# Kernel tuning notes

Hardware: AMD Instinct MI355X
Metric: run time of the kernel (lower is better)

## Reference

```python
import jax, jax.numpy as jnp
import numpy as np

C0, C1, ED, H, L, K = 128, 32, 64, 4, 2, 16
RADIUS = 16.0
EPS = 1e-6


def _ln(x, g, b):
    m = jnp.mean(x, -1, keepdims=True)
    v = jnp.var(x, -1, keepdims=True)
    return (x - m) * jax.lax.rsqrt(v + 1e-5) * g + b


def _gather_nodes(x, idx):
    # x [B,N,...], idx [B,N,K] -> [B,N,K,...]
    return jax.vmap(lambda xb, ib: xb[ib])(x, idx)


def _gather_pairs(e, idx):
    # e [B,N,N,ED], idx [B,N,K] -> [B,N,K,ED]  (batched_index_select on dim=2)
    return jax.vmap(lambda eb, ib: jnp.take_along_axis(eb, ib[..., None], axis=1))(e, idx)


def _fiber_norm(f0, f1, g0, b0, g1, b1):
    # deg-0: LayerNorm + gelu; deg-1: phase-preserving norm on channel magnitudes
    f0n = jax.nn.gelu(_ln(f0, g0, b0))
    n1 = jnp.linalg.norm(f1, axis=-1)                       # [B,N,C1]
    f1n = f1 / (n1 + EPS)[..., None] * jax.nn.gelu(_ln(n1, g1, b1))[..., None]
    return f0n, f1n


def _tfn_kv(f0j, f1j, y1, r, WA, WB):
    # Equivariant TFN edge kernel: paths 0->0(l=0), 1->0(l=1), 0->1(l=1),
    # 1->1(l=0), 1->1(l=1, cross), 1->1(l=2, traceless Y2) with radial gates r.
    r1, r2, r3, r4, r5, r6 = jnp.split(
        r, [C0, C0 + C1, 2 * C0 + C1, 2 * C0 + 2 * C1, 2 * C0 + 3 * C1], axis=-1)
    dot1 = jnp.einsum('bnkcm,bnkm->bnkc', f1j, y1)          # [B,N,K,C1]
    in0 = jnp.concatenate([r1 * f0j, r2 * dot1], -1)        # [B,N,K,C0+C1]
    k0 = jnp.einsum('oc,bnkc->bnko', WA, in0)               # [B,N,K,C0]
    p3 = (r3 * f0j)[..., None] * y1[..., None, :]           # [B,N,K,C0,3]
    p4 = r4[..., None] * f1j
    p5 = r5[..., None] * jnp.cross(f1j, y1[..., None, :])
    p6 = r6[..., None] * (y1[..., None, :] * dot1[..., None] - f1j / 3.0)
    in1 = jnp.concatenate([p3, p4, p5, p6], axis=-2)        # [B,N,K,C0+3*C1,3]
    k1 = jnp.einsum('oc,bnkcm->bnkom', WB, in1)             # [B,N,K,C1,3]
    return k0, k1


def reference(node_feats, pair_feats, coords, eln_g, eln_b, Wi0, Wi1,
              ln0_g, ln0_b, n1_g, n1_b, Wq0, Wq1, WrK, WrV, WkA, WkB, WvA, WvB,
              Wb, Wo0, Wo1, alpha_attn, lnf0_g, lnf0_b, nf1_g, nf1_b,
              Wf0a, Wf0b, Wf1a, Wf1b, alpha_ff, Wp0, Wp1):
    B, N = node_feats.shape[:2]
    Na, CA, Cc, Oo = [coords[..., i, :] for i in range(4)]          # each [B,N,3]
    f1_in = jnp.stack([Na, Cc, Oo], axis=-2) - CA[..., None, :]     # [B,N,3,3]
    # kNN graph on CA coords (exclude self), radius mask at 16A
    d2 = jnp.sum((CA[:, :, None] - CA[:, None, :]) ** 2, -1)        # [B,N,N]
    d2 = d2 + jnp.eye(N, dtype=d2.dtype) * 1e9
    nv, idx = jax.lax.top_k(-d2, K)                                 # idx [B,N,K]
    dist = jnp.sqrt(jnp.maximum(-nv, 0.0))
    mask = dist <= RADIUS
    rel_pos = _gather_nodes(CA, idx) - CA[:, :, None]               # [B,N,K,3]
    rel_b = jax.lax.stop_gradient(rel_pos)                          # basis on detached rel_pos
    y1 = rel_b / (jnp.linalg.norm(rel_b, axis=-1, keepdims=True) + EPS)
    edges = _ln(_gather_pairs(pair_feats, idx), eln_g, eln_b)       # [B,N,K,ED]
    # project in
    f0 = jnp.einsum('oc,bnc->bno', Wi0, node_feats)                 # [B,N,C0]
    f1 = jnp.einsum('oc,bncm->bnom', Wi1, f1_in)                    # [B,N,C1,3]
    dh0, dh1 = C0 // H, C1 // H
    scale = 1.0 / np.sqrt(dh0 + 3 * dh1)
    for l in range(L):
        # ---- attention block (prenorm -> TFN attention -> rezero residual)
        x0, x1 = _fiber_norm(f0, f1, ln0_g[l], ln0_b[l], n1_g[l], n1_b[l])
        q0 = jnp.einsum('oc,bnc->bno', Wq0[l], x0)
        q1 = jnp.einsum('oc,bncm->bnom', Wq1[l], x1)
        x0j = _gather_nodes(x0, idx)                                # [B,N,K,C0]
        x1j = _gather_nodes(x1, idx)                                # [B,N,K,C1,3]
        rk = jnp.einsum('re,bnke->bnkr', WrK[l], edges)
        rv = jnp.einsum('re,bnke->bnkr', WrV[l], edges)
        k0, k1 = _tfn_kv(x0j, x1j, y1, rk, WkA[l], WkB[l])
        v0, v1 = _tfn_kv(x0j, x1j, y1, rv, WvA[l], WvB[l])
        q0h = q0.reshape(B, N, H, dh0)
        q1h = q1.reshape(B, N, H, dh1, 3)
        k0h = k0.reshape(B, N, K, H, dh0)
        k1h = k1.reshape(B, N, K, H, dh1, 3)
        v0h = v0.reshape(B, N, K, H, dh0)
        v1h = v1.reshape(B, N, K, H, dh1, 3)
        logits = (jnp.einsum('bnhc,bnkhc->bnhk', q0h, k0h)
                  + jnp.einsum('bnhcm,bnkhcm->bnhk', q1h, k1h)) * scale
        logits = logits + jnp.einsum('he,bnke->bnhk', Wb[l], edges)
        logits = jnp.where(mask[:, :, None, :], logits, -1e9)
        attn = jax.nn.softmax(logits, axis=-1)
        o0 = jnp.einsum('bnhk,bnkhc->bnhc', attn, v0h).reshape(B, N, C0)
        o1 = jnp.einsum('bnhk,bnkhcm->bnhcm', attn, v1h).reshape(B, N, C1, 3)
        f0 = f0 + alpha_attn[l] * jnp.einsum('oc,bnc->bno', Wo0[l], o0)
        f1 = f1 + alpha_attn[l] * jnp.einsum('oc,bncm->bnom', Wo1[l], o1)
        # ---- fiber feedforward (prenorm -> FF -> rezero residual)
        x0, x1 = _fiber_norm(f0, f1, lnf0_g[l], lnf0_b[l], nf1_g[l], nf1_b[l])
        h0 = jnp.einsum('oh,bnh->bno', Wf0b[l],
                        jax.nn.gelu(jnp.einsum('hc,bnc->bnh', Wf0a[l], x0)))
        h1 = jnp.einsum('hc,bncm->bnhm', Wf1a[l], x1)
        nh = jnp.linalg.norm(h1, axis=-1)
        h1 = h1 * (jax.nn.gelu(nh) / (nh + EPS))[..., None]
        h1 = jnp.einsum('oh,bnhm->bnom', Wf1b[l], h1)
        f0 = f0 + alpha_ff[l] * h0
        f1 = f1 + alpha_ff[l] * h1
    # project out + _to_output
    node_out = jnp.einsum('oc,bnc->bno', Wp0, f0)                   # [B,N,128]
    coords_out = CA[:, :, None, :] + jnp.einsum('oc,bncm->bnom', Wp1, f1)  # [B,N,3,3]
    return node_out, coords_out


def setup_inputs() -> dict:
    key = jax.random.key(0)
    ks = iter(jax.random.split(key, 64))
    def rn(shape, scale=1.0):
        return (jax.random.normal(next(ks), shape) * scale).astype(jnp.float32)
    B, N = 1, 1024
    RC = 2 * C0 + 4 * C1
    ca = jnp.cumsum(rn((B, N, 3), 1.5), axis=1)          # protein-like chain
    coords = ca[:, :, None, :] + rn((B, N, 4, 3), 0.5)
    inp = dict(
        node_feats=rn((B, N, 128)),
        pair_feats=rn((B, N, N, ED)),
        coords=coords,
        eln_g=jnp.ones((ED,), jnp.float32), eln_b=jnp.zeros((ED,), jnp.float32),
        Wi0=rn((C0, 128), 128 ** -0.5), Wi1=rn((C1, 3), 3 ** -0.5),
        ln0_g=jnp.ones((L, C0), jnp.float32), ln0_b=jnp.zeros((L, C0), jnp.float32),
        n1_g=jnp.ones((L, C1), jnp.float32), n1_b=jnp.zeros((L, C1), jnp.float32),
        Wq0=rn((L, C0, C0), C0 ** -0.5), Wq1=rn((L, C1, C1), C1 ** -0.5),
        WrK=rn((L, RC, ED), ED ** -0.5), WrV=rn((L, RC, ED), ED ** -0.5),
        WkA=rn((L, C0, C0 + C1), (C0 + C1) ** -0.5),
        WkB=rn((L, C1, C0 + 3 * C1), (C0 + 3 * C1) ** -0.5),
        WvA=rn((L, C0, C0 + C1), (C0 + C1) ** -0.5),
        WvB=rn((L, C1, C0 + 3 * C1), (C0 + 3 * C1) ** -0.5),
        Wb=rn((L, H, ED), ED ** -0.5),
        Wo0=rn((L, C0, C0), C0 ** -0.5), Wo1=rn((L, C1, C1), C1 ** -0.5),
        alpha_attn=jnp.full((L,), 0.5, jnp.float32),
        lnf0_g=jnp.ones((L, C0), jnp.float32), lnf0_b=jnp.zeros((L, C0), jnp.float32),
        nf1_g=jnp.ones((L, C1), jnp.float32), nf1_b=jnp.zeros((L, C1), jnp.float32),
        Wf0a=rn((L, 4 * C0, C0), C0 ** -0.5), Wf0b=rn((L, C0, 4 * C0), (4 * C0) ** -0.5),
        Wf1a=rn((L, 4 * C1, C1), C1 ** -0.5), Wf1b=rn((L, C1, 4 * C1), (4 * C1) ** -0.5),
        alpha_ff=jnp.full((L,), 0.5, jnp.float32),
        Wp0=rn((128, C0), C0 ** -0.5), Wp1=rn((3, C1), C1 ** -0.5),
    )
    return inp
```

## Files before the change

kernel.cpp:

```cpp
#include <hip/hip_runtime.h>
#include <hip/hip_bf16.h>
#include <math.h>

static constexpr int NN  = 1024;
static constexpr int KK  = 16;
static constexpr int C0c = 128;
static constexpr int C1c = 32;
static constexpr int EDc = 64;
static constexpr int Lc  = 2;
static constexpr int ENUM = NN * KK;
static constexpr int PL   = NN * C1c;
static constexpr int X1HS = NN * 32;
#define SCALE_ATTN 0.13363062095621219f

typedef __attribute__((ext_vector_type(8))) short s8v;
typedef __attribute__((ext_vector_type(4))) float f4v;

__device__ __forceinline__ float wsum64(float v) {
    for (int o = 32; o > 0; o >>= 1) v += __shfl_xor(v, o);
    return v;
}
__device__ __forceinline__ float gsum16(float v) {
    for (int o = 8; o > 0; o >>= 1) v += __shfl_xor(v, o, 16);
    return v;
}
__device__ __forceinline__ float gmax16(float v) {
    for (int o = 8; o > 0; o >>= 1) v = fmaxf(v, __shfl_xor(v, o, 16));
    return v;
}
__device__ __forceinline__ float gelu_f(float x) {
    float x3 = x * x * x;
    return 0.5f * x * (1.0f + tanhf(0.7978845608028654f * (x + 0.044715f * x3)));
}
__device__ __forceinline__ unsigned short f2bf(float x) {
    union { float f; unsigned int u; } v; v.f = x;
    unsigned int r = v.u + 0x7fffu + ((v.u >> 16) & 1u);
    return (unsigned short)(r >> 16);
}
__device__ __forceinline__ float bf2f(unsigned short u) {
    union { float f; unsigned int i; } v; v.i = ((unsigned int)u) << 16;
    return v.f;
}
__device__ __forceinline__ s8v ld8(const unsigned short* p) { return *(const s8v*)p; }
__device__ __forceinline__ f4v mfma16(s8v a, s8v b, f4v c) {
    return __builtin_amdgcn_mfma_f32_16x16x32_bf16(a, b, c, 0, 0, 0);
}

struct CvJob { const float* s; unsigned short* d; int n; };
struct CvJobs { CvJob j[20]; int n; int total; };

__global__ __launch_bounds__(256) void setup_kernel(CvJobs cj, int cvb,
                                                    const float* __restrict__ coords,
                                                    int* __restrict__ idx,
                                                    float* __restrict__ maskf,
                                                    float* __restrict__ y1,
                                                    const float* __restrict__ Wi1,
                                                    float* __restrict__ f1p) {
    __shared__ float ca[NN * 3];
    const int tid = threadIdx.x;
    const int bx = blockIdx.x;
    if (bx < cvb) {
        int g = bx * 256 + tid;
        if (g >= cj.total) return;
        for (int i = 0; i < cj.n; ++i) {
            int n = cj.j[i].n;
            if (g < n) { cj.j[i].d[g] = f2bf(cj.j[i].s[g]); return; }
            g -= n;
        }
        return;
    }
    if (bx < cvb + 256) {
        for (int f = tid; f < NN * 3; f += 256) {
            int i = f / 3, m = f % 3;
            ca[f] = coords[(i * 4 + 1) * 3 + m];
        }
        __syncthreads();
        const int wid = tid >> 6, lane = tid & 63;
        const int n = (bx - cvb) * 4 + wid;
        const float cx = ca[n * 3 + 0], cy = ca[n * 3 + 1], cz = ca[n * 3 + 2];
        float d[16];
#pragma unroll
        for (int s = 0; s < 16; ++s) {
            int i = s * 64 + lane;
            float dx = cx - ca[i * 3 + 0], dy = cy - ca[i * 3 + 1], dz = cz - ca[i * 3 + 2];
            float d2 = dx * dx + dy * dy + dz * dz;
            d[s] = (i == n) ? 1e9f : d2;
        }
        for (int t = 0; t < KK; ++t) {
            float best = 1e30f; int bi = 0;
#pragma unroll
            for (int s = 0; s < 16; ++s) {
                int i = s * 64 + lane;
                float v = d[s];
                if (v < best || (v == best && i < bi)) { best = v; bi = i; }
            }
#pragma unroll
            for (int o = 32; o > 0; o >>= 1) {
                float ov = __shfl_xor(best, o);
                int   oi = __shfl_xor(bi, o);
                if (ov < best || (ov == best && oi < bi)) { best = ov; bi = oi; }
            }
            const int j = bi;
            if (lane == 0) {
                idx[n * KK + t] = j;
                float dist = sqrtf(best);
                maskf[n * KK + t] = (dist <= 16.0f) ? 1.0f : 0.0f;
                float rx = ca[j * 3 + 0] - cx, ry = ca[j * 3 + 1] - cy, rz = ca[j * 3 + 2] - cz;
                float nrm = sqrtf(rx * rx + ry * ry + rz * rz) + 1e-6f;
                y1[(n * KK + t) * 3 + 0] = rx / nrm;
                y1[(n * KK + t) * 3 + 1] = ry / nrm;
                y1[(n * KK + t) * 3 + 2] = rz / nrm;
            }
            const int js = j >> 6, jl = j & 63;
#pragma unroll
            for (int s = 0; s < 16; ++s)
                if (s == js && jl == lane) d[s] = 2e30f;
        }
        return;
    }
    int g = (bx - cvb - 256) * 256 + tid;
    if (g >= NN * 32) return;
    int n = g >> 5, c = g & 31;
    float w0 = Wi1[c * 3 + 0], w1 = Wi1[c * 3 + 1], w2 = Wi1[c * 3 + 2];
#pragma unroll
    for (int m = 0; m < 3; ++m) {
        float cav = coords[(n * 4 + 1) * 3 + m];
        float a0 = coords[(n * 4 + 0) * 3 + m] - cav;
        float a1 = coords[(n * 4 + 2) * 3 + m] - cav;
        float a2 = coords[(n * 4 + 3) * 3 + m] - cav;
        f1p[m * PL + n * 32 + c] = w0 * a0 + w1 * a1 + w2 * a2;
    }
}

__global__ __launch_bounds__(256) void edge_f0_kernel(const float* __restrict__ pair,
                                                      const int* __restrict__ idx,
                                                      const float* __restrict__ g,
                                                      const float* __restrict__ b,
                                                      const float* __restrict__ Wb,
                                                      unsigned short* __restrict__ edges_h,
                                                      float* __restrict__ biasb,
                                                      const unsigned short* __restrict__ nf_h,
                                                      const unsigned short* __restrict__ Wi0_h,
                                                      float* __restrict__ f0) {
    const int t = threadIdx.x, wid = t >> 6, lane = t & 63;
    if (blockIdx.x < ENUM / 4) {
        const int e = blockIdx.x * 4 + wid;
        const int n = e >> 4;
        const int j = idx[e];
        float v = pair[((size_t)n * NN + j) * EDc + lane];
        float m = wsum64(v) * (1.0f / 64.0f);
        float d = v - m;
        float var = wsum64(d * d) * (1.0f / 64.0f);
        float nv = d * rsqrtf(var + 1e-5f) * g[lane] + b[lane];
        edges_h[e * EDc + lane] = f2bf(nv);
#pragma unroll
        for (int l = 0; l < 2; ++l)
#pragma unroll
            for (int h = 0; h < 4; ++h) {
                float tt = wsum64(nv * Wb[(l * 4 + h) * 64 + lane]);
                if (lane == 0) biasb[(size_t)l * ENUM * 4 + e * 4 + h] = tt;
            }
        return;
    }
    int rel = blockIdx.x - ENUM / 4;
    const int mt = rel & 7, ntc = rel >> 3;
    const int m0 = mt * 128 + wid * 32, n0 = ntc * 32;
    const int c16 = lane & 15, g8 = (lane >> 4) * 8, g4 = (lane >> 4) * 4;
    f4v acc[2][2];
#pragma unroll
    for (int a = 0; a < 2; ++a)
#pragma unroll
        for (int bq = 0; bq < 2; ++bq) acc[a][bq] = f4v{0.f, 0.f, 0.f, 0.f};
    const unsigned short* Ap = nf_h + (size_t)(m0 + c16) * 128 + g8;
    const unsigned short* Bp = Wi0_h + (size_t)(n0 + c16) * 128 + g8;
#pragma unroll
    for (int kc = 0; kc < 128; kc += 32) {
        s8v a0 = ld8(Ap + kc);
        s8v a1 = ld8(Ap + 16 * 128 + kc);
        s8v b0 = ld8(Bp + kc);
        s8v b1 = ld8(Bp + 16 * 128 + kc);
        acc[0][0] = mfma16(a0, b0, acc[0][0]);
        acc[0][1] = mfma16(a0, b1, acc[0][1]);
        acc[1][0] = mfma16(a1, b0, acc[1][0]);
        acc[1][1] = mfma16(a1, b1, acc[1][1]);
    }
#pragma unroll
    for (int fm = 0; fm < 2; ++fm)
#pragma unroll
        for (int r = 0; r < 4; ++r) {
            const int m = m0 + fm * 16 + g4 + r;
#pragma unroll
            for (int fn = 0; fn < 2; ++fn)
                f0[(size_t)m * 128 + n0 + fn * 16 + c16] = acc[fm][fn][r];
        }
}

__global__ __launch_bounds__(256) void fnorm1_kernel(const float* __restrict__ f0,
                                                     const float* __restrict__ f1p,
                                                     const float* __restrict__ g0,
                                                     const float* __restrict__ b0,
                                                     const float* __restrict__ g1,
                                                     const float* __restrict__ b1,
                                                     unsigned short* __restrict__ x0h,
                                                     unsigned short* __restrict__ x1h) {
    const int wid = threadIdx.x >> 6, lane = threadIdx.x & 63;
    const int n = blockIdx.x * 4 + wid;
    float va = f0[n * 128 + lane], vb = f0[n * 128 + lane + 64];
    float m = wsum64(va + vb) * (1.0f / 128.0f);
    float da = va - m, db = vb - m;
    float var = wsum64(da * da + db * db) * (1.0f / 128.0f);
    float rs = rsqrtf(var + 1e-5f);
    x0h[n * 128 + lane]      = f2bf(gelu_f(da * rs * g0[lane] + b0[lane]));
    x0h[n * 128 + lane + 64] = f2bf(gelu_f(db * rs * g0[lane + 64] + b0[lane + 64]));
    int c = lane & 31;
    float h0 = f1p[0 * PL + n * 32 + c];
    float h1 = f1p[1 * PL + n * 32 + c];
    float h2 = f1p[2 * PL + n * 32 + c];
    float n1 = sqrtf(h0 * h0 + h1 * h1 + h2 * h2);
    float ms = wsum64(n1) * (1.0f / 64.0f);
    float dd = n1 - ms;
    float vv = wsum64(dd * dd) * (1.0f / 64.0f);
    float sc = gelu_f(dd * rsqrtf(vv + 1e-5f) * g1[c] + b1[c]) / (n1 + 1e-6f);
    if (lane < 32) {
        x1h[0 * X1HS + n * 32 + c] = f2bf(h0 * sc);
        x1h[1 * X1HS + n * 32 + c] = f2bf(h1 * sc);
        x1h[2 * X1HS + n * 32 + c] = f2bf(h2 * sc);
    }
}

static constexpr int LS_IN0 = 0;
static constexpr int LS_INU = 64 * 168;
static constexpr int LS_INW = LS_INU + 64 * 136;
static constexpr int LS_X0  = LS_INW + 3 * 64 * 104;
static constexpr int LS_X1  = LS_X0 + 64 * 128;
static constexpr int LS_Y   = LS_X1 + 3 * 64 * 32;
static constexpr int EKV_LDS2 = LS_Y * 2 + 64 * 3 * 4;

__global__ __launch_bounds__(512) void edge_kv2(
    const unsigned short* __restrict__ edges_h,
    const unsigned short* __restrict__ WrK, const unsigned short* __restrict__ WrV,
    const unsigned short* __restrict__ WkA, const unsigned short* __restrict__ WvA,
    const unsigned short* __restrict__ WkB, const unsigned short* __restrict__ WvB,
    const unsigned short* __restrict__ x0h, const unsigned short* __restrict__ x1h,
    const int* __restrict__ idx, const float* __restrict__ y1,
    unsigned short* __restrict__ k0h, unsigned short* __restrict__ v0h,
    unsigned short* __restrict__ uKh, unsigned short* __restrict__ uVh,
    unsigned short* __restrict__ k1ph, unsigned short* __restrict__ v1ph,
    const unsigned short* __restrict__ Wq0l, const unsigned short* __restrict__ Wq1l,
    float* __restrict__ q0, float* __restrict__ q1p) {
    extern __shared__ unsigned short lsm[];
    const int t = threadIdx.x, w = t >> 6, l = t & 63;
    const int c16 = l & 15, g8 = (l >> 4) * 8, g4 = (l >> 4) * 4;
    const int bid = blockIdx.x;
    if (bid < 256) {
        unsigned short* in0L = lsm + LS_IN0;
        unsigned short* inUL = lsm + LS_INU;
        unsigned short* inWL = lsm + LS_INW;
        unsigned short* x0L  = lsm + LS_X0;
        unsigned short* x1L  = lsm + LS_X1;
        float* yL = (float*)(lsm + LS_Y);
        const int e0 = bid * 64;
        for (int c = t; c < 1024; c += 512) {
            int row = c >> 4, sub = c & 15;
            int j = idx[e0 + row];
            *(s8v*)&x0L[row * 128 + sub * 8] = ld8(x0h + (size_t)j * 128 + sub * 8);
        }
        for (int c = t; c < 768; c += 512) {
            int plane = c >> 8, rem = c & 255;
            int row = rem >> 2, sub = rem & 3;
            int j = idx[e0 + row];
            *(s8v*)&x1L[(plane * 64 + row) * 32 + sub * 8] =
                ld8(x1h + (size_t)plane * X1HS + (size_t)j * 32 + sub * 8);
        }
        if (t < 192) yL[t] = y1[e0 * 3 + t];
        __syncthreads();
#pragma unroll 1
        for (int s = 0; s < 2; ++s) {
            const unsigned short* Wr = s ? WrV : WrK;
            const unsigned short* WA = s ? WvA : WkA;
            const unsigned short* WB = s ? WvB : WkB;
            unsigned short* K0o = s ? v0h : k0h;
            unsigned short* Uo  = s ? uVh : uKh;
            unsigned short* K1o = s ? v1ph : k1ph;
#pragma unroll 1
            for (int ti = w; ti < 24; ti += 8) {
                const int esub = ti & 1, rt = ti >> 1;
                const int e0w = e0 + esub * 32, r0 = rt * 32;
                f4v acc[2][2];
#pragma unroll
                for (int a = 0; a < 2; ++a)
#pragma unroll
                    for (int bq = 0; bq < 2; ++bq) acc[a][bq] = f4v{0.f, 0.f, 0.f, 0.f};
#pragma unroll
                for (int kc = 0; kc < 64; kc += 32) {
                    s8v a0 = ld8(edges_h + (size_t)(e0w + c16) * 64 + kc + g8);
                    s8v a1 = ld8(edges_h + (size_t)(e0w + 16 + c16) * 64 + kc + g8);
                    s8v b0 = ld8(Wr + (size_t)(r0 + c16) * 64 + kc + g8);
                    s8v b1 = ld8(Wr + (size_t)(r0 + 16 + c16) * 64 + kc + g8);
                    acc[0][0] = mfma16(a0, b0, acc[0][0]);
                    acc[0][1] = mfma16(a0, b1, acc[0][1]);
                    acc[1][0] = mfma16(a1, b0, acc[1][0]);
                    acc[1][1] = mfma16(a1, b1, acc[1][1]);
                }
#pragma unroll
                for (int fm = 0; fm < 2; ++fm)
#pragma unroll
                    for (int r = 0; r < 4; ++r) {
                        const int el = esub * 32 + fm * 16 + g4 + r;
                        float ya = yL[el * 3 + 0], yb = yL[el * 3 + 1], yc = yL[el * 3 + 2];
#pragma unroll
                        for (int fn = 0; fn < 2; ++fn) {
                            const float av = acc[fm][fn][r];
                            const int col = r0 + fn * 16 + c16;
                            if (r0 < 128) {
                                in0L[el * 168 + col] = f2bf(av * bf2f(x0L[el * 128 + col]));
                            } else if (r0 < 160) {
                                int c = col - 128;
                                float d1 = bf2f(x1L[(0 * 64 + el) * 32 + c]) * ya
                                         + bf2f(x1L[(1 * 64 + el) * 32 + c]) * yb
                                         + bf2f(x1L[(2 * 64 + el) * 32 + c]) * yc;
                                in0L[el * 168 + col] = f2bf(av * d1);
                            } else if (r0 < 288) {
                                int c = col - 160;
                                inUL[el * 136 + c] = f2bf(av * bf2f(x0L[el * 128 + c]));
                            } else {
                                int c = (r0 < 320) ? (col - 288) : (r0 < 352) ? (col - 320) : (col - 352);
                                float fx = bf2f(x1L[(0 * 64 + el) * 32 + c]);
                                float fy = bf2f(x1L[(1 * 64 + el) * 32 + c]);
                                float fz = bf2f(x1L[(2 * 64 + el) * 32 + c]);
                                float w0, w1, w2; int off;
                                if (r0 < 320) {
                                    off = 0; w0 = av * fx; w1 = av * fy; w2 = av * fz;
                                } else if (r0 < 352) {
                                    off = 32;
                                    w0 = av * (fy * yc - fz * yb);
                                    w1 = av * (fz * ya - fx * yc);
                                    w2 = av * (fx * yb - fy * ya);
                                } else {
                                    off = 64;
                                    float d1 = fx * ya + fy * yb + fz * yc;
                                    w0 = av * (ya * d1 - fx * (1.0f / 3.0f));
                                    w1 = av * (yb * d1 - fy * (1.0f / 3.0f));
                                    w2 = av * (yc * d1 - fz * (1.0f / 3.0f));
                                }
                                inWL[0 * 64 * 104 + el * 104 + off + c] = f2bf(w0);
                                inWL[1 * 64 * 104 + el * 104 + off + c] = f2bf(w1);
                                inWL[2 * 64 * 104 + el * 104 + off + c] = f2bf(w2);
                            }
                        }
                    }
            }
            __syncthreads();
#pragma unroll 1
            for (int ti = w; ti < 16; ti += 8) {
                const unsigned short* Ab; const unsigned short* Bb;
                unsigned short* Cb;
                int apit, K, ldb, ldcq, esub;
                if (ti < 8) {
                    esub = ti & 1; int nt = ti >> 1;
                    Ab = in0L; apit = 168; K = 160;
                    Bb = WA + (size_t)(nt * 32) * 160; ldb = 160;
                    Cb = K0o + (size_t)(e0 + esub * 32) * 128 + nt * 32; ldcq = 128;
                } else if (ti < 10) {
                    esub = ti - 8;
                    Ab = inUL; apit = 136; K = 128; Bb = WB; ldb = 224;
                    Cb = Uo + (size_t)(e0 + esub * 32) * 32; ldcq = 32;
                } else {
                    int id = ti - 10; int m = id >> 1; esub = id & 1;
                    Ab = inWL + m * 64 * 104; apit = 104; K = 96;
                    Bb = WB + 128; ldb = 224;
                    Cb = K1o + ((size_t)m * ENUM + e0 + esub * 32) * 32; ldcq = 32;
                }
                const int m0l = esub * 32;
                f4v acc[2][2];
#pragma unroll
                for (int a = 0; a < 2; ++a)
#pragma unroll
                    for (int bq = 0; bq < 2; ++bq) acc[a][bq] = f4v{0.f, 0.f, 0.f, 0.f};
                for (int kc = 0; kc < K; kc += 32) {
                    s8v a0 = *(const s8v*)&Ab[(m0l + c16) * apit + kc + g8];
                    s8v a1 = *(const s8v*)&Ab[(m0l + 16 + c16) * apit + kc + g8];
                    s8v b0 = ld8(Bb + (size_t)c16 * ldb + kc + g8);
                    s8v b1 = ld8(Bb + (size_t)(16 + c16) * ldb + kc + g8);
                    acc[0][0] = mfma16(a0, b0, acc[0][0]);
                    acc[0][1] = mfma16(a0, b1, acc[0][1]);
                    acc[1][0] = mfma16(a1, b0, acc[1][0]);
                    acc[1][1] = mfma16(a1, b1, acc[1][1]);
                }
#pragma unroll
                for (int fm = 0; fm < 2; ++fm)
#pragma unroll
                    for (int r = 0; r < 4; ++r) {
                        const int lr = fm * 16 + g4 + r;
#pragma unroll
                        for (int fn = 0; fn < 2; ++fn)
                            Cb[(size_t)lr * ldcq + fn * 16 + c16] = f2bf(acc[fm][fn][r]);
                    }
            }
            __syncthreads();
        }
        return;
    }
    const int wt = (bid - 256) * 8 + w;
    const unsigned short* A; const unsigned short* B;
    float* C; int K, lda2, m0, n0, ldc2;
    if (wt < 128) {
        int rowt = wt >> 2, colt = wt & 3;
        A = x0h; B = Wq0l; C = q0;
        K = 128; lda2 = 128; ldc2 = 128;
        m0 = rowt * 32; n0 = colt * 32;
    } else {
        int k = wt - 128;
        int pl = k >> 5, rowt = k & 31;
        A = x1h + (size_t)pl * X1HS; B = Wq1l; C = q1p + (size_t)pl * PL;
        K = 32; lda2 = 32; ldc2 = 32;
        m0 = rowt * 32; n0 = 0;
    }
    f4v acc[2][2];
#pragma unroll
    for (int a = 0; a < 2; ++a)
#pragma unroll
        for (int bq = 0; bq < 2; ++bq) acc[a][bq] = f4v{0.f, 0.f, 0.f, 0.f};
    const unsigned short* Ap = A + (size_t)(m0 + c16) * lda2 + g8;
    const unsigned short* Bp = B + (size_t)(n0 + c16) * lda2 + g8;
    for (int kc = 0; kc < K; kc += 32) {
        s8v a0 = ld8(Ap + kc);
        s8v a1 = ld8(Ap + 16 * lda2 + kc);
        s8v b0 = ld8(Bp + kc);
        s8v b1 = ld8(Bp + 16 * lda2 + kc);
        acc[0][0] = mfma16(a0, b0, acc[0][0]);
        acc[0][1] = mfma16(a0, b1, acc[0][1]);
        acc[1][0] = mfma16(a1, b0, acc[1][0]);
        acc[1][1] = mfma16(a1, b1, acc[1][1]);
    }
#pragma unroll
    for (int fm = 0; fm < 2; ++fm)
#pragma unroll
        for (int r = 0; r < 4; ++r) {
            const int m = m0 + fm * 16 + g4 + r;
#pragma unroll
            for (int fn = 0; fn < 2; ++fn)
                C[(size_t)m * ldc2 + n0 + fn * 16 + c16] = acc[fm][fn][r];
        }
}

__global__ __launch_bounds__(256) void attn_core(const float* __restrict__ q0,
                                                 const float* __restrict__ q1p,
                                                 const unsigned short* __restrict__ k0h,
                                                 const unsigned short* __restrict__ k1ph,
                                                 const unsigned short* __restrict__ v0h,
                                                 const unsigned short* __restrict__ v1ph,
                                                 const unsigned short* __restrict__ uKh,
                                                 const unsigned short* __restrict__ uVh,
                                                 const float* __restrict__ biasb,
                                                 const float* __restrict__ maskf,
                                                 const float* __restrict__ y1,
                                                 unsigned short* __restrict__ o0h,
                                                 unsigned short* __restrict__ o1h) {
    __shared__ float q0s[4][128];
    __shared__ float q1s[4][96];
    __shared__ float attns[4][64];
    const int wid = threadIdx.x >> 6, lane = threadIdx.x & 63;
    const int n = blockIdx.x * 4 + wid;
    q0s[wid][lane]      = q0[n * 128 + lane];
    q0s[wid][lane + 64] = q0[n * 128 + lane + 64];
    if (lane < 32) {
#pragma unroll
        for (int m = 0; m < 3; ++m) q1s[wid][m * 32 + lane] = q1p[m * PL + n * 32 + lane];
    }
    __syncthreads();
    {
        const int h = lane >> 4, k = lane & 15;
        const int e = n * KK + k;
        float acc = 0.f;
        const unsigned short* kr = k0h + (size_t)e * 128 + h * 32;
#pragma unroll
        for (int c8 = 0; c8 < 4; ++c8) {
            s8v kv = ld8(kr + c8 * 8);
#pragma unroll
            for (int j = 0; j < 8; ++j)
                acc += q0s[wid][h * 32 + c8 * 8 + j] * bf2f((unsigned short)kv[j]);
        }
        s8v uv = ld8(uKh + (size_t)e * 32 + h * 8);
#pragma unroll
        for (int m = 0; m < 3; ++m) {
            float yv = y1[e * 3 + m];
            s8v k1v = ld8(k1ph + ((size_t)m * ENUM + e) * 32 + h * 8);
#pragma unroll
            for (int c = 0; c < 8; ++c)
                acc += q1s[wid][m * 32 + h * 8 + c] *
                       (bf2f((unsigned short)k1v[c]) + bf2f((unsigned short)uv[c]) * yv);
        }
        acc = acc * SCALE_ATTN + biasb[e * 4 + h];
        if (maskf[e] == 0.0f) acc = -1e9f;
        float mx = gmax16(acc);
        float ex = expf(acc - mx);
        float sm = gsum16(ex);
        attns[wid][lane] = ex / sm;
    }
    __syncthreads();
    const int g = lane & 15, kq = lane >> 4;
    {
        float o[8] = {};
        const float* aw = &attns[wid][(g >> 2) * 16];
#pragma unroll
        for (int kk2 = 0; kk2 < 4; ++kk2) {
            int kk = kq * 4 + kk2;
            float a = aw[kk];
            s8v v = ld8(v0h + (size_t)(n * KK + kk) * 128 + g * 8);
#pragma unroll
            for (int j = 0; j < 8; ++j) o[j] += a * bf2f((unsigned short)v[j]);
        }
#pragma unroll
        for (int j = 0; j < 8; ++j) {
            o[j] += __shfl_xor(o[j], 16);
            o[j] += __shfl_xor(o[j], 32);
        }
        if (kq == 0) {
            s8v r;
#pragma unroll
            for (int j = 0; j < 8; ++j) r[j] = (short)f2bf(o[j]);
            *(s8v*)&o0h[(size_t)n * 128 + g * 8] = r;
        }
    }
    {
        float o[8] = {};
        const int plane = g >> 2, cg = g & 3;
        if (g < 12) {
            const float* aw = &attns[wid][cg * 16];
#pragma unroll
            for (int kk2 = 0; kk2 < 4; ++kk2) {
                int kk = kq * 4 + kk2;
                int e2 = n * KK + kk;
                float a = aw[kk];
                float yv = y1[e2 * 3 + plane];
                s8v v = ld8(v1ph + ((size_t)plane * ENUM + e2) * 32 + cg * 8);
                s8v u = ld8(uVh + (size_t)e2 * 32 + cg * 8);
#pragma unroll
                for (int j = 0; j < 8; ++j)
                    o[j] += a * (bf2f((unsigned short)v[j]) + bf2f((unsigned short)u[j]) * yv);
            }
        }
#pragma unroll
        for (int j = 0; j < 8; ++j) {
            o[j] += __shfl_xor(o[j], 16);
            o[j] += __shfl_xor(o[j], 32);
        }
        if (kq == 0 && g < 12) {
            s8v r;
#pragma unroll
            for (int j = 0; j < 8; ++j) r[j] = (short)f2bf(o[j]);
            *(s8v*)&o1h[((size_t)plane * NN + n) * 32 + cg * 8] = r;
        }
    }
}

template <int MODE>
__global__ __launch_bounds__(512) void fused_post(
    const unsigned short* __restrict__ o0h, const unsigned short* __restrict__ o1h,
    float* __restrict__ f0, float* __restrict__ f1p,
    const unsigned short* __restrict__ Wo0h, const unsigned short* __restrict__ Wo1h,
    const unsigned short* __restrict__ Wf0ah, const unsigned short* __restrict__ Wf0bh,
    const unsigned short* __restrict__ Wf1ah, const unsigned short* __restrict__ Wf1bh,
    const float* __restrict__ alA, const float* __restrict__ alF,
    const float* __restrict__ lnf0_g, const float* __restrict__ lnf0_b,
    const float* __restrict__ nf1_g, const float* __restrict__ nf1_b,
    const float* __restrict__ ln0n_g, const float* __restrict__ ln0n_b,
    const float* __restrict__ n1n_g, const float* __restrict__ n1n_b,
    unsigned short* __restrict__ x0h, unsigned short* __restrict__ x1h,
    const unsigned short* __restrict__ Wp0h, const float* __restrict__ Wp1,
    const float* __restrict__ coords, float* __restrict__ out) {
    __shared__ float f0s[16][132];
    __shared__ float f1s[3][16][36];
    __shared__ unsigned short x0s[16][136];
    __shared__ float x1s[3][16][36];
    __shared__ unsigned short hs[16][520];
    __shared__ unsigned short h1b[3][16][136];
    const int t = threadIdx.x, w = t >> 6, l = t & 63;
    const int c16 = l & 15, g8 = (l >> 4) * 8, g4 = (l >> 4) * 4;
    const int n0 = blockIdx.x * 16;
    const float aA = alA[0], aF = alF[0];

    {
        f4v acc = f4v{0.f, 0.f, 0.f, 0.f};
        const unsigned short* Ap = o0h + (size_t)(n0 + c16) * 128 + g8;
#pragma unroll
        for (int kc = 0; kc < 128; kc += 32) {
            s8v a = ld8(Ap + kc);
            s8v b = ld8(Wo0h + (size_t)(w * 16 + c16) * 128 + g8 + kc);
            acc = mfma16(a, b, acc);
        }
        int colg = w * 16 + c16;
#pragma unroll
        for (int r = 0; r < 4; ++r) {
            int row = g4 + r;
            f0s[row][colg] = f0[(size_t)(n0 + row) * 128 + colg] + aA * acc[r];
        }
    }
#pragma unroll
    for (int it = 0; it < 3; ++it) {
        int g = t + it * 512;
        int c = g & 31, node = (g >> 5) & 15, m = g >> 9;
        float a = 0.f;
        const unsigned short* wrow = Wo1h + c * 32;
        const unsigned short* orow = o1h + ((size_t)m * NN + n0 + node) * 32;
#pragma unroll
        for (int cc = 0; cc < 32; ++cc) a += bf2f(wrow[cc]) * bf2f(orow[cc]);
        f1s[m][node][c] = f1p[(size_t)m * PL + (n0 + node) * 32 + c] + aA * a;
    }
    __syncthreads();
    for (int i = 0; i < 2; ++i) {
        int row = w * 2 + i;
        float v0 = f0s[row][l], v1 = f0s[row][l + 64];
        float mn = wsum64(v0 + v1) * (1.0f / 128.0f);
        float d0 = v0 - mn, d1 = v1 - mn;
        float var = wsum64(d0 * d0 + d1 * d1) * (1.0f / 128.0f);
        float rs = rsqrtf(var + 1e-5f);
        x0s[row][l]      = f2bf(gelu_f(d0 * rs * lnf0_g[l] + lnf0_b[l]));
        x0s[row][l + 64] = f2bf(gelu_f(d1 * rs * lnf0_g[l + 64] + lnf0_b[l + 64]));
    }
    if (t < 256) {
        int node = t >> 4, sub = t & 15;
        float p[2][3], n1v[2];
#pragma unroll
        for (int q = 0; q < 2; ++q) {
            int c = sub + q * 16;
            p[q][0] = f1s[0][node][c]; p[q][1] = f1s[1][node][c]; p[q][2] = f1s[2][node][c];
            n1v[q] = sqrtf(p[q][0]*p[q][0] + p[q][1]*p[q][1] + p[q][2]*p[q][2]);
        }
        float s = gsum16(n1v[0] + n1v[1]);
        float mn = s * (1.0f / 32.0f);
        float d0 = n1v[0] - mn, d1 = n1v[1] - mn;
        float vv = gsum16(d0 * d0 + d1 * d1);
        float rs = rsqrtf(vv * (1.0f / 32.0f) + 1e-5f);
#pragma unroll
        for (int q = 0; q < 2; ++q) {
            int c = sub + q * 16;
            float sc = gelu_f((n1v[q] - mn) * rs * nf1_g[c] + nf1_b[c]) / (n1v[q] + 1e-6f);
            x1s[0][node][c] = p[q][0] * sc;
            x1s[1][node][c] = p[q][1] * sc;
            x1s[2][node][c] = p[q][2] * sc;
        }
    }
    __syncthreads();
    {
        f4v acc[4];
#pragma unroll
        for (int i = 0; i < 4; ++i) acc[i] = f4v{0.f,0.f,0.f,0.f};
#pragma unroll
        for (int kc = 0; kc < 128; kc += 32) {
            s8v a = *(const s8v*)&x0s[c16][kc + g8];
#pragma unroll
            for (int tt = 0; tt < 4; ++tt) {
                s8v b = ld8(Wf0ah + (size_t)((w * 4 + tt) * 16 + c16) * 128 + g8 + kc);
                acc[tt] = mfma16(a, b, acc[tt]);
            }
        }
#pragma unroll
        for (int tt = 0; tt < 4; ++tt) {
            int colg = (w * 4 + tt) * 16 + c16;
#pragma unroll
            for (int r = 0; r < 4; ++r) hs[g4 + r][colg] = f2bf(gelu_f(acc[tt][r]));
        }
    }
#pragma unroll
    for (int it = 0; it < 4; ++it) {
        int g = t + it * 512;
        int r = g & 127, node = g >> 7;
        float a0 = 0.f, a1 = 0.f, a2 = 0.f;
        const unsigned short* wrow = Wf1ah + r * 32;
#pragma unroll
        for (int c = 0; c < 32; ++c) {
            float wv = bf2f(wrow[c]);
            a0 += wv * x1s[0][node][c];
            a1 += wv * x1s[1][node][c];
            a2 += wv * x1s[2][node][c];
        }
        float nh = sqrtf(a0 * a0 + a1 * a1 + a2 * a2);
        float sc = gelu_f(nh) / (nh + 1e-6f);
        h1b[0][node][r] = f2bf(a0 * sc);
        h1b[1][node][r] = f2bf(a1 * sc);
        h1b[2][node][r] = f2bf(a2 * sc);
    }
    __syncthreads();
    {
        f4v acc = f4v{0.f, 0.f, 0.f, 0.f};
#pragma unroll 4
        for (int kc = 0; kc < 512; kc += 32) {
            s8v a = *(const s8v*)&hs[c16][kc + g8];
            s8v b = ld8(Wf0bh + (size_t)(w * 16 + c16) * 512 + g8 + kc);
            acc = mfma16(a, b, acc);
        }
        int colg = w * 16 + c16;
#pragma unroll
        for (int r = 0; r < 4; ++r) {
            int row = g4 + r;
            float v = f0s[row][colg] + aF * acc[r];
            f0s[row][colg] = v;
            f0[(size_t)(n0 + row) * 128 + colg] = v;
        }
    }
#pragma unroll
    for (int it = 0; it < 3; ++it) {
        int g = t + it * 512;
        int c = g & 31, node = (g >> 5) & 15, m = g >> 9;
        float a = 0.f;
        const unsigned short* wrow = Wf1bh + c * 128;
#pragma unroll 8
        for (int r = 0; r < 128; ++r) a += bf2f(wrow[r]) * bf2f(h1b[m][node][r]);
        float v = f1s[m][node][c] + aF * a;
        f1s[m][node][c] = v;
        f1p[(size_t)m * PL + (n0 + node) * 32 + c] = v;
    }
    __syncthreads();
    if (MODE == 0) {
        for (int i = 0; i < 2; ++i) {
            int row = w * 2 + i;
            float v0 = f0s[row][l], v1 = f0s[row][l + 64];
            float mn = wsum64(v0 + v1) * (1.0f / 128.0f);
            float d0 = v0 - mn, d1 = v1 - mn;
            float var = wsum64(d0 * d0 + d1 * d1) * (1.0f / 128.0f);
            float rs = rsqrtf(var + 1e-5f);
            x0h[(size_t)(n0 + row) * 128 + l]      = f2bf(gelu_f(d0 * rs * ln0n_g[l] + ln0n_b[l]));
            x0h[(size_t)(n0 + row) * 128 + l + 64] = f2bf(gelu_f(d1 * rs * ln0n_g[l + 64] + ln0n_b[l + 64]));
        }
        if (t < 256) {
            int node = t >> 4, sub = t & 15;
            float p[2][3], n1v[2];
#pragma unroll
            for (int q = 0; q < 2; ++q) {
                int c = sub + q * 16;
                p[q][0] = f1s[0][node][c]; p[q][1] = f1s[1][node][c]; p[q][2] = f1s[2][node][c];
                n1v[q] = sqrtf(p[q][0]*p[q][0] + p[q][1]*p[q][1] + p[q][2]*p[q][2]);
            }
            float s = gsum16(n1v[0] + n1v[1]);
            float mn = s * (1.0f / 32.0f);
            float d0 = n1v[0] - mn, d1 = n1v[1] - mn;
            float vv = gsum16(d0 * d0 + d1 * d1);
            float rs = rsqrtf(vv * (1.0f / 32.0f) + 1e-5f);
#pragma unroll
            for (int q = 0; q < 2; ++q) {
                int c = sub + q * 16;
                float sc = gelu_f((n1v[q] - mn) * rs * n1n_g[c] + n1n_b[c]) / (n1v[q] + 1e-6f);
                x1h[(size_t)0 * X1HS + (n0 + node) * 32 + c] = f2bf(p[q][0] * sc);
                x1h[(size_t)1 * X1HS + (n0 + node) * 32 + c] = f2bf(p[q][1] * sc);
                x1h[(size_t)2 * X1HS + (n0 + node) * 32 + c] = f2bf(p[q][2] * sc);
            }
        }
    } else {
#pragma unroll
        for (int it = 0; it < 4; ++it) {
            int g = t + it * 512;
            int row = g >> 7, col = g & 127;
            x0s[row][col] = f2bf(f0s[row][col]);
        }
        __syncthreads();
        f4v acc = f4v{0.f, 0.f, 0.f, 0.f};
#pragma unroll
        for (int kc = 0; kc < 128; kc += 32) {
            s8v a = *(const s8v*)&x0s[c16][kc + g8];
            s8v b = ld8(Wp0h + (size_t)(w * 16 + c16) * 128 + g8 + kc);
            acc = mfma16(a, b, acc);
        }
        int colg = w * 16 + c16;
#pragma unroll
        for (int r = 0; r < 4; ++r)
            out[(size_t)(n0 + g4 + r) * 128 + colg] = acc[r];
        if (t < 144) {
            int node = t / 9, rr = t % 9, o = rr / 3, m = rr % 3;
            float a = coords[((size_t)(n0 + node) * 4 + 1) * 3 + m];
            for (int c = 0; c < 32; ++c) a += Wp1[o * 32 + c] * f1s[m][node][c];
            out[NN * 128 + ((size_t)(n0 + node) * 3 + o) * 3 + m] = a;
        }
    }
}

extern "C" void kernel_launch(void* const* d_in, const int* in_sizes, int n_in,
                              void* d_out, int out_size, void* d_ws, size_t ws_size,
                              hipStream_t stream) {
    (void)in_sizes; (void)n_in; (void)out_size; (void)ws_size;
    const float* node_feats = (const float*)d_in[0];
    const float* pair       = (const float*)d_in[1];
    const float* coords     = (const float*)d_in[2];
    const float* eln_g      = (const float*)d_in[3];
    const float* eln_b      = (const float*)d_in[4];
    const float* Wi0        = (const float*)d_in[5];
    const float* Wi1        = (const float*)d_in[6];
    const float* ln0_g      = (const float*)d_in[7];
    const float* ln0_b      = (const float*)d_in[8];
    const float* n1_g       = (const float*)d_in[9];
    const float* n1_b       = (const float*)d_in[10];
    const float* Wq0        = (const float*)d_in[11];
    const float* Wq1        = (const float*)d_in[12];
    const float* WrK        = (const float*)d_in[13];
    const float* WrV        = (const float*)d_in[14];
    const float* WkA        = (const float*)d_in[15];
    const float* WkB        = (const float*)d_in[16];
    const float* WvA        = (const float*)d_in[17];
    const float* WvB        = (const float*)d_in[18];
    const float* Wb         = (const float*)d_in[19];
    const float* Wo0        = (const float*)d_in[20];
    const float* Wo1        = (const float*)d_in[21];
    const float* alpha_attn = (const float*)d_in[22];
    const float* lnf0_g     = (const float*)d_in[23];
    const float* lnf0_b     = (const float*)d_in[24];
    const float* nf1_g      = (const float*)d_in[25];
    const float* nf1_b      = (const float*)d_in[26];
    const float* Wf0a       = (const float*)d_in[27];
    const float* Wf0b       = (const float*)d_in[28];
    const float* Wf1a       = (const float*)d_in[29];
    const float* Wf1b       = (const float*)d_in[30];
    const float* alpha_ff   = (const float*)d_in[31];
    const float* Wp0        = (const float*)d_in[32];
    const float* Wp1        = (const float*)d_in[33];
    float* out = (float*)d_out;

    float* ws = (float*)d_ws;
    size_t off = 0;
    int*   idx   = (int*)(ws + off); off += NN * KK;
    float* maskf = ws + off;         off += NN * KK;
    float* y1    = ws + off;         off += NN * KK * 3;
    float* f0    = ws + off;         off += NN * C0c;
    float* f1p   = ws + off;         off += 3 * PL;
    float* q0    = ws + off;         off += NN * C0c;
    float* q1p   = ws + off;         off += 3 * PL;
    float* biasb = ws + off;         off += (size_t)2 * ENUM * 4;
    off = (off + 3) & ~(size_t)3;
    unsigned short* up = (unsigned short*)(ws + off);
    size_t uo = 0;
    unsigned short* edges_h = up + uo; uo += (size_t)ENUM * 64;
    unsigned short* x0h     = up + uo; uo += (size_t)NN * 128;
    unsigned short* x1h     = up + uo; uo += (size_t)3 * X1HS;
    unsigned short* nf_h    = up + uo; uo += (size_t)NN * 128;
    unsigned short* k0h     = up + uo; uo += (size_t)ENUM * 128;
    unsigned short* v0h     = up + uo; uo += (size_t)ENUM * 128;
    unsigned short* uKh     = up + uo; uo += (size_t)ENUM * 32;
    unsigned short* uVh     = up + uo; uo += (size_t)ENUM * 32;
    unsigned short* k1ph    = up + uo; uo += (size_t)3 * ENUM * 32;
    unsigned short* v1ph    = up + uo; uo += (size_t)3 * ENUM * 32;
    unsigned short* o0h     = up + uo; uo += (size_t)NN * 128;
    unsigned short* o1h     = up + uo; uo += (size_t)3 * NN * 32;
    unsigned short* WrK_h   = up + uo; uo += 2 * 24576;
    unsigned short* WrV_h   = up + uo; uo += 2 * 24576;
    unsigned short* WkA_h   = up + uo; uo += 2 * 20480;
    unsigned short* WvA_h   = up + uo; uo += 2 * 20480;
    unsigned short* WkB_h   = up + uo; uo += 2 * 7168;
    unsigned short* WvB_h   = up + uo; uo += 2 * 7168;
    unsigned short* Wq0_h   = up + uo; uo += 2 * 16384;
    unsigned short* Wq1_h   = up + uo; uo += 2 * 1024;
    unsigned short* Wo0_h   = up + uo; uo += 2 * 16384;
    unsigned short* Wo1_h   = up + uo; uo += 2 * 1024;
    unsigned short* Wf0a_h  = up + uo; uo += 2 * 65536;
    unsigned short* Wf0b_h  = up + uo; uo += 2 * 65536;
    unsigned short* Wf1a_h  = up + uo; uo += 2 * 4096;
    unsigned short* Wf1b_h  = up + uo; uo += 2 * 4096;
    unsigned short* Wp0_h   = up + uo; uo += 16384;
    unsigned short* Wi0_h   = up + uo; uo += 16384;

    CvJobs cj; cj.n = 17;
    cj.j[0]  = {WrK,  WrK_h,  2 * 24576};
    cj.j[1]  = {WrV,  WrV_h,  2 * 24576};
    cj.j[2]  = {WkA,  WkA_h,  2 * 20480};
    cj.j[3]  = {WvA,  WvA_h,  2 * 20480};
    cj.j[4]  = {WkB,  WkB_h,  2 * 7168};
    cj.j[5]  = {WvB,  WvB_h,  2 * 7168};
    cj.j[6]  = {Wq0,  Wq0_h,  2 * 16384};
    cj.j[7]  = {Wq1,  Wq1_h,  2 * 1024};
    cj.j[8]  = {Wo0,  Wo0_h,  2 * 16384};
    cj.j[9]  = {Wo1,  Wo1_h,  2 * 1024};
    cj.j[10] = {Wf0a, Wf0a_h, 2 * 65536};
    cj.j[11] = {Wf0b, Wf0b_h, 2 * 65536};
    cj.j[12] = {Wf1a, Wf1a_h, 2 * 4096};
    cj.j[13] = {Wf1b, Wf1b_h, 2 * 4096};
    cj.j[14] = {Wp0,  Wp0_h,  16384};
    cj.j[15] = {Wi0,  Wi0_h,  16384};
    cj.j[16] = {node_feats, nf_h, NN * 128};
    cj.total = 2*24576*2 + 2*20480*2 + 2*7168*2 + 2*16384 + 2*1024 + 2*16384
             + 2*1024 + 2*65536*2 + 2*4096*2 + 16384 + 16384 + NN*128;
    const int cvb = (cj.total + 255) / 256;

    setup_kernel<<<cvb + 256 + 128, 256, 0, stream>>>(cj, cvb, coords, idx, maskf, y1, Wi1, f1p);
    edge_f0_kernel<<<ENUM / 4 + 32, 256, 0, stream>>>(pair, idx, eln_g, eln_b, Wb,
                                                      edges_h, biasb, nf_h, Wi0_h, f0);
    fnorm1_kernel<<<NN / 4, 256, 0, stream>>>(f0, f1p, ln0_g, ln0_b, n1_g, n1_b, x0h, x1h);

    for (int l = 0; l < Lc; ++l) {
        edge_kv2<<<284, 512, EKV_LDS2, stream>>>(
            edges_h,
            WrK_h + (size_t)l * 24576, WrV_h + (size_t)l * 24576,
            WkA_h + (size_t)l * 20480, WvA_h + (size_t)l * 20480,
            WkB_h + (size_t)l * 7168,  WvB_h + (size_t)l * 7168,
            x0h, x1h, idx, y1,
            k0h, v0h, uKh, uVh, k1ph, v1ph,
            Wq0_h + (size_t)l * 16384, Wq1_h + (size_t)l * 1024, q0, q1p);
        attn_core<<<NN / 4, 256, 0, stream>>>(q0, q1p, k0h, k1ph, v0h, v1ph, uKh, uVh,
            biasb + (size_t)l * ENUM * 4, maskf, y1, o0h, o1h);
        if (l == 0) {
            fused_post<0><<<NN / 16, 512, 0, stream>>>(
                o0h, o1h, f0, f1p,
                Wo0_h, Wo1_h, Wf0a_h, Wf0b_h, Wf1a_h, Wf1b_h,
                alpha_attn + 0, alpha_ff + 0,
                lnf0_g, lnf0_b, nf1_g, nf1_b,
                ln0_g + 128, ln0_b + 128, n1_g + 32, n1_b + 32,
                x0h, x1h, nullptr, nullptr, nullptr, nullptr);
        } else {
            fused_post<1><<<NN / 16, 512, 0, stream>>>(
                o0h, o1h, f0, f1p,
                Wo0_h + 16384, Wo1_h + 1024, Wf0a_h + 65536, Wf0b_h + 65536,
                Wf1a_h + 4096, Wf1b_h + 4096,
                alpha_attn + 1, alpha_ff + 1,
                lnf0_g + 128, lnf0_b + 128, nf1_g + 32, nf1_b + 32,
                nullptr, nullptr, nullptr, nullptr,
                nullptr, nullptr, Wp0_h, Wp1, coords, out);
        }
    }
}
```

Before: 229.7 us.

## Move attention bias projection into edge_kv kernel as MFMA; stage edges in LDS

The per-layer attention bias (edge features times Wb) is no longer computed in edge_f0_kernel with eight 64-lane shuffle reductions per edge. It is now computed inside edge_kv2 with MFMA, using two extra warp tiles whose weight operand is zero-padded from 4 to 16 columns, and the bias buffer shrinks to one layer and is reused. The edge feature tile is also staged once into LDS with padded rows instead of being reloaded from global memory for every radial tile. This removes shuffle-heavy work and redundant global loads, at the cost of more LDS per block and slightly uneven warp work in the second loop.

```diff
diff --git a/kernel.cpp b/kernel.cpp
--- a/kernel.cpp
+++ b/kernel.cpp
@@ -136,9 +136,7 @@
                                                       const int* __restrict__ idx,
                                                       const float* __restrict__ g,
                                                       const float* __restrict__ b,
-                                                      const float* __restrict__ Wb,
                                                       unsigned short* __restrict__ edges_h,
-                                                      float* __restrict__ biasb,
                                                       const unsigned short* __restrict__ nf_h,
                                                       const unsigned short* __restrict__ Wi0_h,
                                                       float* __restrict__ f0) {
@@ -153,13 +151,6 @@
         float var = wsum64(d * d) * (1.0f / 64.0f);
         float nv = d * rsqrtf(var + 1e-5f) * g[lane] + b[lane];
         edges_h[e * EDc + lane] = f2bf(nv);
-#pragma unroll
-        for (int l = 0; l < 2; ++l)
-#pragma unroll
-            for (int h = 0; h < 4; ++h) {
-                float tt = wsum64(nv * Wb[(l * 4 + h) * 64 + lane]);
-                if (lane == 0) biasb[(size_t)l * ENUM * 4 + e * 4 + h] = tt;
-            }
         return;
     }
     int rel = blockIdx.x - ENUM / 4;
@@ -233,7 +224,8 @@
 static constexpr int LS_INW = LS_INU + 64 * 136;
 static constexpr int LS_X0  = LS_INW + 3 * 64 * 104;
 static constexpr int LS_X1  = LS_X0 + 64 * 128;
-static constexpr int LS_Y   = LS_X1 + 3 * 64 * 32;
+static constexpr int LS_ED  = LS_X1 + 3 * 64 * 32;
+static constexpr int LS_Y   = LS_ED + 64 * 72;
 static constexpr int EKV_LDS2 = LS_Y * 2 + 64 * 3 * 4;
 
 __global__ __launch_bounds__(512) void edge_kv2(
@@ -241,11 +233,13 @@
     const unsigned short* __restrict__ WrK, const unsigned short* __restrict__ WrV,
     const unsigned short* __restrict__ WkA, const unsigned short* __restrict__ WvA,
     const unsigned short* __restrict__ WkB, const unsigned short* __restrict__ WvB,
+    const unsigned short* __restrict__ WbL,
     const unsigned short* __restrict__ x0h, const unsigned short* __restrict__ x1h,
     const int* __restrict__ idx, const float* __restrict__ y1,
     unsigned short* __restrict__ k0h, unsigned short* __restrict__ v0h,
     unsigned short* __restrict__ uKh, unsigned short* __restrict__ uVh,
     unsigned short* __restrict__ k1ph, unsigned short* __restrict__ v1ph,
+    float* __restrict__ biasb,
     const unsigned short* __restrict__ Wq0l, const unsigned short* __restrict__ Wq1l,
     float* __restrict__ q0, float* __restrict__ q1p) {
     extern __shared__ unsigned short lsm[];
@@ -258,6 +252,7 @@
         unsigned short* inWL = lsm + LS_INW;
         unsigned short* x0L  = lsm + LS_X0;
         unsigned short* x1L  = lsm + LS_X1;
+        unsigned short* edL  = lsm + LS_ED;
         float* yL = (float*)(lsm + LS_Y);
         const int e0 = bid * 64;
         for (int c = t; c < 1024; c += 512) {
@@ -271,6 +266,10 @@
             int j = idx[e0 + row];
             *(s8v*)&x1L[(plane * 64 + row) * 32 + sub * 8] =
                 ld8(x1h + (size_t)plane * X1HS + (size_t)j * 32 + sub * 8);
+        }
+        for (int c = t; c < 512; c += 512) {
+            int row = c >> 3, sub = c & 7;
+            *(s8v*)&edL[row * 72 + sub * 8] = ld8(edges_h + (size_t)(e0 + row) * 64 + sub * 8);
         }
         if (t < 192) yL[t] = y1[e0 * 3 + t];
         __syncthreads();
@@ -285,7 +284,7 @@
 #pragma unroll 1
             for (int ti = w; ti < 24; ti += 8) {
                 const int esub = ti & 1, rt = ti >> 1;
-                const int e0w = e0 + esub * 32, r0 = rt * 32;
+                const int el0 = esub * 32, r0 = rt * 32;
                 f4v acc[2][2];
 #pragma unroll
                 for (int a = 0; a < 2; ++a)
@@ -293,8 +292,8 @@
                     for (int bq = 0; bq < 2; ++bq) acc[a][bq] = f4v{0.f, 0.f, 0.f, 0.f};
 #pragma unroll
                 for (int kc = 0; kc < 64; kc += 32) {
-                    s8v a0 = ld8(edges_h + (size_t)(e0w + c16) * 64 + kc + g8);
-                    s8v a1 = ld8(edges_h + (size_t)(e0w + 16 + c16) * 64 + kc + g8);
+                    s8v a0 = *(const s8v*)&edL[(el0 + c16) * 72 + kc + g8];
+                    s8v a1 = *(const s8v*)&edL[(el0 + 16 + c16) * 72 + kc + g8];
                     s8v b0 = ld8(Wr + (size_t)(r0 + c16) * 64 + kc + g8);
                     s8v b1 = ld8(Wr + (size_t)(r0 + 16 + c16) * 64 + kc + g8);
                     acc[0][0] = mfma16(a0, b0, acc[0][0]);
@@ -306,7 +305,7 @@
                 for (int fm = 0; fm < 2; ++fm)
 #pragma unroll
                     for (int r = 0; r < 4; ++r) {
-                        const int el = esub * 32 + fm * 16 + g4 + r;
+                        const int el = el0 + fm * 16 + g4 + r;
                         float ya = yL[el * 3 + 0], yb = yL[el * 3 + 1], yc = yL[el * 3 + 2];
 #pragma unroll
                         for (int fn = 0; fn < 2; ++fn) {
@@ -351,8 +350,32 @@
                     }
             }
             __syncthreads();
+            const int tmax = (s == 0) ? 18 : 16;
 #pragma unroll 1
-            for (int ti = w; ti < 16; ti += 8) {
+            for (int ti = w; ti < tmax; ti += 8) {
+                if (ti >= 16) {
+                    const int esub = ti - 16;
+                    f4v bacc[2] = {f4v{0.f,0.f,0.f,0.f}, f4v{0.f,0.f,0.f,0.f}};
+                    s8v zb;
+#pragma unroll
+                    for (int j = 0; j < 8; ++j) zb[j] = 0;
+#pragma unroll
+                    for (int kc = 0; kc < 64; kc += 32) {
+                        s8v a0 = *(const s8v*)&edL[(esub * 32 + c16) * 72 + kc + g8];
+                        s8v a1 = *(const s8v*)&edL[(esub * 32 + 16 + c16) * 72 + kc + g8];
+                        s8v b0 = (c16 < 4) ? ld8(WbL + (size_t)c16 * 64 + kc + g8) : zb;
+                        bacc[0] = mfma16(a0, b0, bacc[0]);
+                        bacc[1] = mfma16(a1, b0, bacc[1]);
+                    }
+                    if (c16 < 4) {
+#pragma unroll
+                        for (int fm = 0; fm < 2; ++fm)
+#pragma unroll
+                            for (int r = 0; r < 4; ++r)
+                                biasb[(size_t)(e0 + esub * 32 + fm * 16 + g4 + r) * 4 + c16] = bacc[fm][r];
+                    }
+                    continue;
+                }
                 const unsigned short* Ab; const unsigned short* Bb;
                 unsigned short* Cb;
                 int apit, K, ldb, ldcq, esub;
@@ -824,7 +847,7 @@
     float* f1p   = ws + off;         off += 3 * PL;
     float* q0    = ws + off;         off += NN * C0c;
     float* q1p   = ws + off;         off += 3 * PL;
-    float* biasb = ws + off;         off += (size_t)2 * ENUM * 4;
+    float* biasb = ws + off;         off += (size_t)ENUM * 4;
     off = (off + 3) & ~(size_t)3;
     unsigned short* up = (unsigned short*)(ws + off);
     size_t uo = 0;
@@ -856,8 +879,9 @@
     unsigned short* Wf1b_h  = up + uo; uo += 2 * 4096;
     unsigned short* Wp0_h   = up + uo; uo += 16384;
     unsigned short* Wi0_h   = up + uo; uo += 16384;
-
-    CvJobs cj; cj.n = 17;
+    unsigned short* Wb_h    = up + uo; uo += 2 * 256;
+
+    CvJobs cj; cj.n = 18;
     cj.j[0]  = {WrK,  WrK_h,  2 * 24576};
     cj.j[1]  = {WrV,  WrV_h,  2 * 24576};
     cj.j[2]  = {WkA,  WkA_h,  2 * 20480};
@@ -875,13 +899,14 @@
     cj.j[14] = {Wp0,  Wp0_h,  16384};
     cj.j[15] = {Wi0,  Wi0_h,  16384};
     cj.j[16] = {node_feats, nf_h, NN * 128};
+    cj.j[17] = {Wb,   Wb_h,   2 * 256};
     cj.total = 2*24576*2 + 2*20480*2 + 2*7168*2 + 2*16384 + 2*1024 + 2*16384
-             + 2*1024 + 2*65536*2 + 2*4096*2 + 16384 + 16384 + NN*128;
+             + 2*1024 + 2*65536*2 + 2*4096*2 + 16384 + 16384 + NN*128 + 2*256;
     const int cvb = (cj.total + 255) / 256;
 
     setup_kernel<<<cvb + 256 + 128, 256, 0, stream>>>(cj, cvb, coords, idx, maskf, y1, Wi1, f1p);
-    edge_f0_kernel<<<ENUM / 4 + 32, 256, 0, stream>>>(pair, idx, eln_g, eln_b, Wb,
-                                                      edges_h, biasb, nf_h, Wi0_h, f0);
+    edge_f0_kernel<<<ENUM / 4 + 32, 256, 0, stream>>>(pair, idx, eln_g, eln_b,
+                                                      edges_h, nf_h, Wi0_h, f0);
     fnorm1_kernel<<<NN / 4, 256, 0, stream>>>(f0, f1p, ln0_g, ln0_b, n1_g, n1_b, x0h, x1h);
 
     for (int l = 0; l < Lc; ++l) {
@@ -890,11 +915,12 @@
             WrK_h + (size_t)l * 24576, WrV_h + (size_t)l * 24576,
             WkA_h + (size_t)l * 20480, WvA_h + (size_t)l * 20480,
             WkB_h + (size_t)l * 7168,  WvB_h + (size_t)l * 7168,
+            Wb_h + (size_t)l * 256,
             x0h, x1h, idx, y1,
-            k0h, v0h, uKh, uVh, k1ph, v1ph,
+            k0h, v0h, uKh, uVh, k1ph, v1ph, biasb,
             Wq0_h + (size_t)l * 16384, Wq1_h + (size_t)l * 1024, q0, q1p);
         attn_core<<<NN / 4, 256, 0, stream>>>(q0, q1p, k0h, k1ph, v0h, v1ph, uKh, uVh,
-            biasb + (size_t)l * ENUM * 4, maskf, y1, o0h, o1h);
+            biasb, maskf, y1, o0h, o1h);
         if (l == 0) {
             fused_post<0><<<NN / 16, 512, 0, stream>>>(
                 o0h, o1h, f0, f1p,
```

Result: faster. 219.0 us (median of 2 runs) (-4.7%).
